# Optimization experiments

Hardware: AMD Instinct MI355X
Metric: run time of the kernel (lower is better)

The kernel has to match this reference:

```python
import jax, jax.numpy as jnp
import numpy as np

N = 100000
E = 3200000
D = 256
HOPS = 3  # K + 1


def setup_inputs() -> dict:
    key = jax.random.key(0)
    k1, k2, k3, k4, k5 = jax.random.split(key, 5)
    node_features = jax.random.normal(k1, (N, D), dtype=jnp.float32)
    # glorot-uniform-like scale for K+1 Dense kernels
    limit = np.sqrt(6.0 / (D + D)).astype(np.float32)
    W = jax.random.uniform(k2, (HOPS, D, D), dtype=jnp.float32, minval=-limit, maxval=limit)
    adj_vals = jax.random.uniform(k3, (HOPS, E), dtype=jnp.float32)
    adj_rows = jax.random.randint(k4, (HOPS, E), 0, N, dtype=jnp.int32)
    adj_cols = jax.random.randint(k5, (HOPS, E), 0, N, dtype=jnp.int32)
    return {"node_features": node_features, "W": W, "adj_vals": adj_vals,
            "adj_rows": adj_rows, "adj_cols": adj_cols}


def reference(node_features, W, adj_vals, adj_rows, adj_cols):
    """Faithful eval-mode forward: sum over hops of SpMM(A_hop, X @ W_hop), then ReLU.
    Dropout is identity at inference (training=False)."""
    n = node_features.shape[0]
    out = jnp.zeros((n, W.shape[-1]), dtype=node_features.dtype)
    for hop in range(W.shape[0]):  # small fixed K+1 loop, structurally distinct hops
        feats = node_features @ W[hop]                      # [N, out_dim]
        msgs = adj_vals[hop][:, None] * feats[adj_cols[hop]]  # gather + scale, [E, out_dim]
        out = out + jax.ops.segment_sum(msgs, adj_rows[hop], num_segments=n)
    return jax.nn.relu(out)
```

## Files before the change

kernel.cpp:

```cpp
#include <hip/hip_runtime.h>

#define D 256
#define MAXB 128
#define SR 1024
#define PCH 32768

typedef __attribute__((ext_vector_type(8))) short short8;
typedef __attribute__((ext_vector_type(4))) float f32x4;

__device__ __forceinline__ ushort f2b(float f) {
    unsigned u = __float_as_uint(f);
    u += 0x7fffu + ((u >> 16) & 1u);
    return (ushort)(u >> 16);
}
__device__ __forceinline__ float b2f(ushort h) {
    return __uint_as_float(((unsigned)h) << 16);
}
__device__ __forceinline__ long long ntload_ll(const void* p) {
    return __builtin_nontemporal_load((const long long*)p);
}

__global__ void xconv_kernel(const float* __restrict__ X, ushort* __restrict__ Xb, int total8) {
    int i = blockIdx.x * 256 + threadIdx.x;
    if (i >= total8) return;
    const float4 a = *(const float4*)(X + (size_t)i * 8);
    const float4 b = *(const float4*)(X + (size_t)i * 8 + 4);
    ushort o8[8] = {f2b(a.x), f2b(a.y), f2b(a.z), f2b(a.w),
                    f2b(b.x), f2b(b.y), f2b(b.z), f2b(b.w)};
    *(short8*)(Xb + (size_t)i * 8) = *(const short8*)o8;
}

__global__ void wconv_kernel(const float* __restrict__ W, ushort* __restrict__ WT, int total) {
    int idx = blockIdx.x * 256 + threadIdx.x;
    if (idx >= total) return;
    int h = idx >> 16;
    int c = (idx >> 8) & 255, k = idx & 255;
    WT[(h << 16) + c * 256 + k] = f2b(W[(h << 16) + k * 256 + c]);
}

__global__ __launch_bounds__(512) void bpart_kernel(const int* __restrict__ rows,
                                                    const int* __restrict__ cols,
                                                    const float* __restrict__ vals,
                                                    int2* __restrict__ raw,
                                                    int* __restrict__ runofs,
                                                    int e, int nbuk, int nch) {
    __shared__ int lh[MAXB];
    __shared__ int lcur[MAXB];
    int h = blockIdx.y, c = blockIdx.x;
    int c0 = c * PCH, c1 = min(c0 + PCH, e);
    if (c0 >= c1) return;
    const int*   rr = rows + (size_t)h * e;
    const int*   cc = cols + (size_t)h * e;
    const float* vv = vals + (size_t)h * e;
    int tid = threadIdx.x;
    for (int k = tid; k < nbuk; k += 512) { lh[k] = 0; lcur[k] = 0; }
    __syncthreads();
    for (int i = c0 + tid; i < c1; i += 512)
        atomicAdd(&lh[rr[i] >> 10], 1);
    __syncthreads();
    int* ro = runofs + (size_t)(h * nch + c) * (nbuk + 1);
    if (tid == 0) {
        int run = h * e + c0;
        for (int j = 0; j < nbuk; ++j) {
            ro[j] = run;
            int v = lh[j];
            lh[j] = run;
            run += v;
        }
        ro[nbuk] = h * e + c1;
    }
    __syncthreads();
    for (int i = c0 + tid; i < c1; i += 512) {
        int row = rr[i];
        int b = row >> 10;
        int p = lh[b] + atomicAdd(&lcur[b], 1);
        raw[p] = make_int2(cc[i] | ((row & 1023) << 17), __float_as_int(vv[i]));
    }
}

__global__ __launch_bounds__(128) void bsum_kernel(const int* __restrict__ runofs,
                                                   int* __restrict__ tot, int nbuk, int nch) {
    int key = blockIdx.x;
    int h = key / nbuk, b = key % nbuk;
    int tid = threadIdx.x;
    int sum = 0;
    for (int c = tid; c < nch; c += 128) {
        const int* ro = runofs + (size_t)(h * nch + c) * (nbuk + 1) + b;
        sum += ro[1] - ro[0];
    }
    #pragma unroll
    for (int o = 32; o > 0; o >>= 1) sum += __shfl_xor(sum, o);
    __shared__ int ws_[2];
    if ((tid & 63) == 0) ws_[tid >> 6] = sum;
    __syncthreads();
    if (tid == 0) tot[key] = ws_[0] + ws_[1];
}

__global__ __launch_bounds__(1024) void bscan_kernel(const int* __restrict__ tot,
                                                     int* __restrict__ gbase, int total) {
    __shared__ int s[1024];
    int t = threadIdx.x;
    int C = (total + 1023) >> 10;
    int i0 = t * C, i1 = min(i0 + C, total);
    int sum = 0;
    for (int i = i0; i < i1; ++i) sum += tot[i];
    s[t] = sum;
    __syncthreads();
    for (int off = 1; off < 1024; off <<= 1) {
        int x = (t >= off) ? s[t - off] : 0;
        __syncthreads();
        s[t] += x;
        __syncthreads();
    }
    int run = s[t] - sum;
    for (int i = i0; i < i1; ++i) {
        gbase[i] = run;
        run += tot[i];
    }
    if (t == 1023) gbase[total] = s[1023];
}

__global__ __launch_bounds__(512) void bsort_kernel(const int* __restrict__ gbase,
                                                    const int* __restrict__ runofs,
                                                    const int2* __restrict__ raw,
                                                    int2* __restrict__ eg,
                                                    int* __restrict__ row_ptr,
                                                    int n, int nbuk, int nch) {
    __shared__ int hist[1024];
    __shared__ int ss[512];
    __shared__ int cur[1024];
    int key = blockIdx.x;
    int h = key / nbuk, b = key % nbuk;
    int s = gbase[key], t = gbase[key + 1];
    int tid = threadIdx.x;
    hist[tid] = 0; hist[tid + 512] = 0;
    __syncthreads();
    for (int c = 0; c < nch; ++c) {
        const int* ro = runofs + (size_t)(h * nch + c) * (nbuk + 1) + b;
        int rs = ro[0], re = ro[1];
        for (int i = rs + tid; i < re; i += 512)
            atomicAdd(&hist[(((unsigned)raw[i].x) >> 17) & 1023], 1);
    }
    __syncthreads();
    int a = hist[2 * tid], c2 = hist[2 * tid + 1];
    int pair = a + c2;
    ss[tid] = pair;
    __syncthreads();
    for (int off = 1; off < 512; off <<= 1) {
        int x = (tid >= off) ? ss[tid - off] : 0;
        __syncthreads();
        ss[tid] += x;
        __syncthreads();
    }
    int excl = s + ss[tid] - pair;
    cur[2 * tid] = excl;
    cur[2 * tid + 1] = excl + a;
    int* rp = row_ptr + (size_t)h * (n + 1);
    int grow = b * SR + 2 * tid;
    if (grow < n)     rp[grow]     = excl;
    if (grow + 1 < n) rp[grow + 1] = excl + a;
    if (tid == 0 && b == nbuk - 1) rp[n] = t;
    __syncthreads();
    for (int c = 0; c < nch; ++c) {
        const int* ro = runofs + (size_t)(h * nch + c) * (nbuk + 1) + b;
        int rs = ro[0], re = ro[1];
        for (int i = rs + tid; i < re; i += 512) {
            int2 ev = raw[i];
            int j = (((unsigned)ev.x) >> 17) & 1023;
            int p = atomicAdd(&cur[j], 1);
            eg[p] = ev;
        }
    }
}

__global__ __launch_bounds__(256) void spmmX_kernel(const int* __restrict__ row_ptr,
                                                    const int2* __restrict__ eg,
                                                    const ushort* __restrict__ Xb,
                                                    ushort* __restrict__ Y, int n,
                                                    size_t rpStride, size_t yStride) {
    const int* rp = row_ptr + blockIdx.y * rpStride;
    ushort* Yh = Y + blockIdx.y * yStride;
    int w = threadIdx.x >> 6, lane = threadIdx.x & 63;
    int r = blockIdx.x * 4 + w;
    if (r >= n) return;
    int g = lane >> 4, l4 = lane & 15;
    int doff = l4 * 16;
    const ushort* xb = Xb + doff;
    int e0 = rp[r], e1 = rp[r + 1];
    float acc[16] = {};

    int i0 = e0 + g;
    long long d_cur = (i0 < e1) ? ntload_ll(eg + i0) : 0;
    int c_cur = ((int)(unsigned)d_cur) & 0x1FFFF;
    short8 va = *(const short8*)(xb + (size_t)c_cur * 256);
    short8 vb = *(const short8*)(xb + (size_t)c_cur * 256 + 8);
    int i1 = e0 + 4 + g;
    long long d_nxt = (i1 < e1) ? ntload_ll(eg + i1) : 0;

    for (int ee = e0; ee < e1; ee += 4) {
        int c_nxt = ((int)(unsigned)d_nxt) & 0x1FFFF;
        short8 wa = *(const short8*)(xb + (size_t)c_nxt * 256);
        short8 wb = *(const short8*)(xb + (size_t)c_nxt * 256 + 8);
        int i2 = ee + 8 + g;
        long long d_n2 = (i2 < e1) ? ntload_ll(eg + i2) : 0;

        float val = __int_as_float((int)(d_cur >> 32));
        #pragma unroll
        for (int i = 0; i < 8; ++i)
            acc[i] = fmaf(val, b2f((ushort)va[i]), acc[i]);
        #pragma unroll
        for (int i = 0; i < 8; ++i)
            acc[8 + i] = fmaf(val, b2f((ushort)vb[i]), acc[8 + i]);

        d_cur = d_nxt; va = wa; vb = wb; d_nxt = d_n2;
    }
    #pragma unroll
    for (int i = 0; i < 16; ++i) acc[i] += __shfl_xor(acc[i], 16);
    #pragma unroll
    for (int i = 0; i < 16; ++i) acc[i] += __shfl_xor(acc[i], 32);
    if (g == 0) {
        union { ushort u[16]; long long ll[4]; } o;
        #pragma unroll
        for (int i = 0; i < 16; ++i) o.u[i] = f2b(acc[i]);
        long long* dst = (long long*)(Yh + (size_t)r * 256 + doff);
        __builtin_nontemporal_store(o.ll[0], dst);
        __builtin_nontemporal_store(o.ll[1], dst + 1);
        __builtin_nontemporal_store(o.ll[2], dst + 2);
        __builtin_nontemporal_store(o.ll[3], dst + 3);
    }
}

#define BP 40

__global__ __launch_bounds__(256) void gemmY2_kernel(const ushort* __restrict__ Y,
                                                     const ushort* __restrict__ WT,
                                                     float* __restrict__ out, int M,
                                                     int nh, int hoff, int mode) {
    __shared__ ushort As[64 * BP];
    __shared__ ushort Bs[256 * BP];
    int tid = threadIdx.x;
    int r0 = blockIdx.x * 64;
    int w = tid >> 6, lane = tid & 63;
    int lo = lane & 15, hi = lane >> 4;
    f32x4 acc[16] = {};

    int srow = tid >> 2;
    int skq = (tid & 3) * 8;
    int arow = r0 + srow; if (arow > M - 1) arow = M - 1;

    for (int ks = 0; ks < nh * 8; ++ks) {
        int hh = ks >> 3, k0 = (ks & 7) * 32;
        short8 av = *(const short8*)(Y + ((size_t)hh * M + arow) * 256 + k0 + skq);
        const ushort* bp = WT + ((size_t)(hoff + hh) << 16) + (size_t)tid * 256 + k0;
        short8 bv0 = *(const short8*)(bp);
        short8 bv1 = *(const short8*)(bp + 8);
        short8 bv2 = *(const short8*)(bp + 16);
        short8 bv3 = *(const short8*)(bp + 24);
        __syncthreads();
        *(short8*)&As[srow * BP + skq] = av;
        *(short8*)&Bs[tid * BP +  0] = bv0;
        *(short8*)&Bs[tid * BP +  8] = bv1;
        *(short8*)&Bs[tid * BP + 16] = bv2;
        *(short8*)&Bs[tid * BP + 24] = bv3;
        __syncthreads();
        short8 a = *(const short8*)&As[(w * 16 + lo) * BP + hi * 8];
        #pragma unroll
        for (int j = 0; j < 16; ++j) {
            short8 bf = *(const short8*)&Bs[(j * 16 + lo) * BP + hi * 8];
            acc[j] = __builtin_amdgcn_mfma_f32_16x16x32_bf16(a, bf, acc[j], 0, 0, 0);
        }
    }
    #pragma unroll
    for (int j = 0; j < 16; ++j)
        #pragma unroll
        for (int i = 0; i < 4; ++i) {
            int row = r0 + w * 16 + hi * 4 + i;
            int col = j * 16 + lo;
            if (row < M) {
                float v = acc[j][i];
                float* op = &out[(size_t)row * 256 + col];
                if (mode & 1) v += *op;
                if (mode & 2) v = fmaxf(v, 0.f);
                *op = v;
            }
        }
}

extern "C" void kernel_launch(void* const* d_in, const int* in_sizes, int n_in,
                              void* d_out, int out_size, void* d_ws, size_t ws_size,
                              hipStream_t stream) {
    const float* X    = (const float*)d_in[0];
    const float* W    = (const float*)d_in[1];
    const float* vals = (const float*)d_in[2];
    const int*   rows = (const int*)d_in[3];
    const int*   cols = (const int*)d_in[4];
    int n    = in_sizes[0] / D;
    int hops = in_sizes[1] / (D * D);
    int e    = in_sizes[2] / hops;

    int nbuk    = (n + SR - 1) / SR;
    int nkeytot = hops * nbuk;
    int nch     = (e + PCH - 1) / PCH;

    float* out = (float*)d_out;

    auto padded = [](size_t b) { return (b + 255) & ~(size_t)255; };
    char* wsb = (char*)d_ws;
    size_t off = 0;
    auto alloc = [&](size_t bytes) -> void* { void* p = wsb + off; off += padded(bytes); return p; };

    ushort* WT      = (ushort*)alloc((size_t)hops * D * D * 2);
    ushort* Xb      = (ushort*)alloc((size_t)n * D * 2);
    int*    runofs  = (int*)   alloc((size_t)hops * nch * (nbuk + 1) * 4);
    int*    tot     = (int*)   alloc((size_t)nkeytot * 4);
    int*    gbase   = (int*)   alloc((size_t)(nkeytot + 1) * 4);
    int*    row_ptr = (int*)   alloc((size_t)hops * (n + 1) * 4);
    int2*   edges   = (int2*)  alloc((size_t)hops * e * 8);
    size_t  raw_off = off;
    int2*   raw     = (int2*)  alloc((size_t)hops * e * 8);

    bool bigY = (ws_size >= raw_off + (size_t)hops * n * D * 2);
    ushort* Y = (ushort*)raw;

    xconv_kernel<<<(n * D / 8 + 255) / 256, 256, 0, stream>>>(X, Xb, n * D / 8);
    wconv_kernel<<<(hops * D * D + 255) / 256, 256, 0, stream>>>(W, WT, hops * D * D);

    bpart_kernel<<<dim3(nch, hops), 512, 0, stream>>>(rows, cols, vals, raw, runofs, e, nbuk, nch);
    bsum_kernel<<<nkeytot, 128, 0, stream>>>(runofs, tot, nbuk, nch);
    bscan_kernel<<<1, 1024, 0, stream>>>(tot, gbase, nkeytot);
    bsort_kernel<<<nkeytot, 512, 0, stream>>>(gbase, runofs, raw, edges, row_ptr, n, nbuk, nch);

    if (bigY) {
        spmmX_kernel<<<dim3((n + 3) / 4, hops), 256, 0, stream>>>(row_ptr, edges, Xb, Y, n,
                                                                  (size_t)(n + 1), (size_t)n * D);
        gemmY2_kernel<<<(n + 63) / 64, 256, 0, stream>>>(Y, WT, out, n, hops, 0, 2);
    } else {
        for (int h = 0; h < hops; ++h) {
            spmmX_kernel<<<dim3((n + 3) / 4, 1), 256, 0, stream>>>(row_ptr + (size_t)h * (n + 1),
                                                                   edges, Xb, Y, n, 0, 0);
            int mode = (h > 0 ? 1 : 0) | (h == hops - 1 ? 2 : 0);
            gemmY2_kernel<<<(n + 63) / 64, 256, 0, stream>>>(Y, WT, out, n, 1, h, mode);
        }
    }
}
```

Measured before the change: 1.132 ms.

## Fuse bucket-sum into scan, halve partition chunks, per-wave run scanning in bsort

Halves the partition chunk size so bpart launches more blocks. The separate bucket-sum kernel is folded into the single-block scan, where each thread sums its own key's run lengths, saving a launch and a buffer. In bsort, each wave now walks whole chunk runs with a 64-lane stride instead of the whole block sweeping each short run with a 512-lane stride, which should cut idle lanes now that runs are short. The costs are more runofs entries to read and a fused scan that only works when hops*nbuk fits in 1024 threads; the per-thread serial loop over nch in the scan may also be slower.

```diff
diff --git a/kernel.cpp b/kernel.cpp
--- a/kernel.cpp
+++ b/kernel.cpp
@@ -3,7 +3,7 @@
 #define D 256
 #define MAXB 128
 #define SR 1024
-#define PCH 32768
+#define PCH 16384
 
 typedef __attribute__((ext_vector_type(8))) short short8;
 typedef __attribute__((ext_vector_type(4))) float f32x4;
@@ -78,32 +78,19 @@
     }
 }
 
-__global__ __launch_bounds__(128) void bsum_kernel(const int* __restrict__ runofs,
-                                                   int* __restrict__ tot, int nbuk, int nch) {
-    int key = blockIdx.x;
-    int h = key / nbuk, b = key % nbuk;
-    int tid = threadIdx.x;
-    int sum = 0;
-    for (int c = tid; c < nch; c += 128) {
-        const int* ro = runofs + (size_t)(h * nch + c) * (nbuk + 1) + b;
-        sum += ro[1] - ro[0];
-    }
-    #pragma unroll
-    for (int o = 32; o > 0; o >>= 1) sum += __shfl_xor(sum, o);
-    __shared__ int ws_[2];
-    if ((tid & 63) == 0) ws_[tid >> 6] = sum;
-    __syncthreads();
-    if (tid == 0) tot[key] = ws_[0] + ws_[1];
-}
-
-__global__ __launch_bounds__(1024) void bscan_kernel(const int* __restrict__ tot,
-                                                     int* __restrict__ gbase, int total) {
+__global__ __launch_bounds__(1024) void bscan_kernel(const int* __restrict__ runofs,
+                                                     int* __restrict__ gbase,
+                                                     int nbuk, int nch, int nkeytot) {
     __shared__ int s[1024];
     int t = threadIdx.x;
-    int C = (total + 1023) >> 10;
-    int i0 = t * C, i1 = min(i0 + C, total);
     int sum = 0;
-    for (int i = i0; i < i1; ++i) sum += tot[i];
+    if (t < nkeytot) {
+        int h = t / nbuk, b = t % nbuk;
+        for (int c = 0; c < nch; ++c) {
+            const int* ro = runofs + (size_t)(h * nch + c) * (nbuk + 1) + b;
+            sum += ro[1] - ro[0];
+        }
+    }
     s[t] = sum;
     __syncthreads();
     for (int off = 1; off < 1024; off <<= 1) {
@@ -112,12 +99,8 @@
         s[t] += x;
         __syncthreads();
     }
-    int run = s[t] - sum;
-    for (int i = i0; i < i1; ++i) {
-        gbase[i] = run;
-        run += tot[i];
-    }
-    if (t == 1023) gbase[total] = s[1023];
+    if (t < nkeytot) gbase[t] = s[t] - sum;
+    if (t == nkeytot - 1) gbase[nkeytot] = s[t];
 }
 
 __global__ __launch_bounds__(512) void bsort_kernel(const int* __restrict__ gbase,
@@ -133,12 +116,13 @@
     int h = key / nbuk, b = key % nbuk;
     int s = gbase[key], t = gbase[key + 1];
     int tid = threadIdx.x;
+    int w = tid >> 6, lane = tid & 63;
     hist[tid] = 0; hist[tid + 512] = 0;
     __syncthreads();
-    for (int c = 0; c < nch; ++c) {
+    for (int c = w; c < nch; c += 8) {
         const int* ro = runofs + (size_t)(h * nch + c) * (nbuk + 1) + b;
         int rs = ro[0], re = ro[1];
-        for (int i = rs + tid; i < re; i += 512)
+        for (int i = rs + lane; i < re; i += 64)
             atomicAdd(&hist[(((unsigned)raw[i].x) >> 17) & 1023], 1);
     }
     __syncthreads();
@@ -161,10 +145,10 @@
     if (grow + 1 < n) rp[grow + 1] = excl + a;
     if (tid == 0 && b == nbuk - 1) rp[n] = t;
     __syncthreads();
-    for (int c = 0; c < nch; ++c) {
+    for (int c = w; c < nch; c += 8) {
         const int* ro = runofs + (size_t)(h * nch + c) * (nbuk + 1) + b;
         int rs = ro[0], re = ro[1];
-        for (int i = rs + tid; i < re; i += 512) {
+        for (int i = rs + lane; i < re; i += 64) {
             int2 ev = raw[i];
             int j = (((unsigned)ev.x) >> 17) & 1023;
             int p = atomicAdd(&cur[j], 1);
@@ -312,7 +296,6 @@
     ushort* WT      = (ushort*)alloc((size_t)hops * D * D * 2);
     ushort* Xb      = (ushort*)alloc((size_t)n * D * 2);
     int*    runofs  = (int*)   alloc((size_t)hops * nch * (nbuk + 1) * 4);
-    int*    tot     = (int*)   alloc((size_t)nkeytot * 4);
     int*    gbase   = (int*)   alloc((size_t)(nkeytot + 1) * 4);
     int*    row_ptr = (int*)   alloc((size_t)hops * (n + 1) * 4);
     int2*   edges   = (int2*)  alloc((size_t)hops * e * 8);
@@ -326,8 +309,7 @@
     wconv_kernel<<<(hops * D * D + 255) / 256, 256, 0, stream>>>(W, WT, hops * D * D);
 
     bpart_kernel<<<dim3(nch, hops), 512, 0, stream>>>(rows, cols, vals, raw, runofs, e, nbuk, nch);
-    bsum_kernel<<<nkeytot, 128, 0, stream>>>(runofs, tot, nbuk, nch);
-    bscan_kernel<<<1, 1024, 0, stream>>>(tot, gbase, nkeytot);
+    bscan_kernel<<<1, 1024, 0, stream>>>(runofs, gbase, nbuk, nch, nkeytot);
     bsort_kernel<<<nkeytot, 512, 0, stream>>>(gbase, runofs, raw, edges, row_ptr, n, nbuk, nch);
 
     if (bigY) {
```

New measurement: 1.136 ms. About the same (+0.4%).
